# Optimization experiments

Hardware: AMD Instinct MI355X
Metric: run time of the kernel (lower is better)

Reference implementation:

```python
import jax, jax.numpy as jnp
import numpy as np

B, H, W, C, HEADS = 8, 64, 64, 128, 4
H_SP, W_SP = 64, 8            # idx=0: H_sp = H, W_sp = split_size
HD = C // HEADS               # 32
N = H_SP * W_SP               # 512 tokens per window
SCALE = HD ** -0.5


def setup_inputs() -> dict:
    key = jax.random.key(0)
    k1, k2, k3 = jax.random.split(key, 3)
    return {
        "qkv": jax.random.normal(k1, (3, B, H * W, C), dtype=jnp.float32),
        "conv_w": jax.random.normal(k2, (C, 1, 3, 3), dtype=jnp.float32) * 0.1,
        "conv_b": jax.random.normal(k3, (C,), dtype=jnp.float32) * 0.1,
    }


def _to_windows(x):
    # x: [B, L, C] -> window tokens [Bw, N, C] with Bw = B * (H//H_SP) * (W//W_SP)
    x = x.reshape(B, H // H_SP, H_SP, W // W_SP, W_SP, C)
    x = x.transpose(0, 1, 3, 2, 4, 5).reshape(-1, N, C)
    return x


def _heads(x):
    # [Bw, N, C] -> [Bw, heads, N, hd]
    return x.reshape(-1, N, HEADS, HD).transpose(0, 2, 1, 3)


def reference(qkv, conv_w, conv_b):
    q, k, v = qkv[0], qkv[1], qkv[2]

    qw = _heads(_to_windows(q)) * SCALE   # [Bw, h, N, hd]
    kw = _heads(_to_windows(k))

    vwin = _to_windows(v)                 # [Bw, N, C]
    # LePE: depthwise 3x3 conv on each window (NHWC, feature_group_count=C)
    vimg = vwin.reshape(-1, H_SP, W_SP, C)
    w_hwio = conv_w.transpose(2, 3, 1, 0)  # [3,3,1,C]
    lepe = jax.lax.conv_general_dilated(
        vimg, w_hwio, window_strides=(1, 1), padding='SAME',
        dimension_numbers=('NHWC', 'HWIO', 'NHWC'), feature_group_count=C,
    ) + conv_b
    lepe = _heads(lepe.reshape(-1, N, C))  # [Bw, h, N, hd]
    vw = _heads(vwin)

    attn = jax.nn.softmax(jnp.einsum('whqd,whkd->whqk', qw, kw), axis=-1)
    out = jnp.einsum('whqk,whkd->whqd', attn, vw) + lepe  # [Bw, h, N, hd]

    # merge heads and windows back to [B, L, C]
    out = out.transpose(0, 2, 1, 3).reshape(-1, N, C)
    out = out.reshape(B, H // H_SP, W // W_SP, H_SP, W_SP, C)
    out = out.transpose(0, 1, 3, 2, 4, 5).reshape(B, H * W, C)
    return out
```

## Files before the change

kernel.cpp:

```cpp
#include <hip/hip_runtime.h>


namespace {
constexpr int Bn   = 8;
constexpr int Ww   = 64;
constexpr int Cc   = 128;
constexpr int HD   = 32;
constexpr int WSP  = 8;
constexpr int NTOK = 512;
constexpr int LL   = 64 * 64;
constexpr float SCALE_L2E = 0.17677669529663687f * 1.4426950408889634f;
constexpr int KPAD = 40;
constexpr int VPAD = 536;
}

typedef __bf16 bf16x8 __attribute__((ext_vector_type(8)));
typedef float  f32x16 __attribute__((ext_vector_type(16)));
typedef unsigned int uint32x4 __attribute__((ext_vector_type(4)));

__device__ inline unsigned cvtpk(float x, float y) {
    unsigned r;
    asm("v_cvt_pk_bf16_f32 %0, %1, %2" : "=v"(r) : "v"(x), "v"(y));
    return r;
}

__global__ __launch_bounds__(1024, 4) void attn_kernel(const float* __restrict__ qkv,
                                                       const float* __restrict__ cw,
                                                       const float* __restrict__ cb,
                                                       float* __restrict__ out) {
    const int blk = blockIdx.x;
    const int w   = blk >> 2;
    const int h   = blk & 3;
    const int b   = w >> 3;
    const int wb  = w & 7;
    const int tid = threadIdx.x;
    const int wv  = tid >> 6;
    const int lane = tid & 63;
    const int l31 = lane & 31;
    const int h5  = lane >> 5;

    const float* qp = qkv;
    const float* kp = qkv + (size_t)Bn * LL * Cc;
    const float* vp = qkv + (size_t)2 * Bn * LL * Cc;

    __shared__ short K_lds[NTOK][KPAD];
    __shared__ short VT_lds[HD][VPAD];

    const int qtok = wv * 32 + l31;
    const int qlqi = (qtok >> 3) * Ww + wb * WSP + (qtok & 7);
    bf16x8 qf[2];
    {
        const float* p = qp + ((size_t)b * LL + qlqi) * Cc + h * HD + h5 * 8;
#pragma unroll
        for (int dc = 0; dc < 2; ++dc) {
            float4 a = *reinterpret_cast<const float4*>(p + dc * 16);
            float4 c = *reinterpret_cast<const float4*>(p + dc * 16 + 4);
            uint32x4 u;
            u.x = cvtpk(a.x * SCALE_L2E, a.y * SCALE_L2E);
            u.y = cvtpk(a.z * SCALE_L2E, a.w * SCALE_L2E);
            u.z = cvtpk(c.x * SCALE_L2E, c.y * SCALE_L2E);
            u.w = cvtpk(c.z * SCALE_L2E, c.w * SCALE_L2E);
            qf[dc] = __builtin_bit_cast(bf16x8, u);
        }
    }

    for (int i = tid; i < (NTOK / 2) * 8; i += 1024) {
        const int tp = i >> 3, j = i & 7;
        const int t0 = tp * 2, t1 = t0 + 1;
        const int lqi0 = (t0 >> 3) * Ww + wb * WSP + (t0 & 7);
        const size_t b0 = ((size_t)b * LL + lqi0) * Cc + h * HD + j * 4;
        const float4 k0 = *reinterpret_cast<const float4*>(kp + b0);
        const float4 k1 = *reinterpret_cast<const float4*>(kp + b0 + Cc);
        uint2 pk0, pk1;
        pk0.x = cvtpk(k0.x, k0.y);  pk0.y = cvtpk(k0.z, k0.w);
        pk1.x = cvtpk(k1.x, k1.y);  pk1.y = cvtpk(k1.z, k1.w);
        *reinterpret_cast<uint2*>(&K_lds[t0][j * 4]) = pk0;
        *reinterpret_cast<uint2*>(&K_lds[t1][j * 4]) = pk1;
        const float4 v0 = *reinterpret_cast<const float4*>(vp + b0);
        const float4 v1 = *reinterpret_cast<const float4*>(vp + b0 + Cc);
        *reinterpret_cast<unsigned*>(&VT_lds[j * 4 + 0][t0]) = cvtpk(v0.x, v1.x);
        *reinterpret_cast<unsigned*>(&VT_lds[j * 4 + 1][t0]) = cvtpk(v0.y, v1.y);
        *reinterpret_cast<unsigned*>(&VT_lds[j * 4 + 2][t0]) = cvtpk(v0.z, v1.z);
        *reinterpret_cast<unsigned*>(&VT_lds[j * 4 + 3][t0]) = cvtpk(v0.w, v1.w);
    }
    __syncthreads();

    f32x16 acc = (f32x16)(0.f);
    float lsum = 0.f;
    const f32x16 z16 = (f32x16)(0.f);

    auto load_kf = [&](int kt, bf16x8* kf) {
        const int krow = kt * 32 + l31;
#pragma unroll
        for (int dc = 0; dc < 2; ++dc)
            kf[dc] = __builtin_bit_cast(bf16x8,
                *reinterpret_cast<const uint32x4*>(&K_lds[krow][dc * 16 + h5 * 8]));
    };

    bf16x8 kf[2];
    load_kf(0, kf);

    for (int kt = 0; kt < 16; ++kt) {
        __builtin_amdgcn_s_setprio(1);
        f32x16 s = z16;
        s = __builtin_amdgcn_mfma_f32_32x32x16_bf16(kf[0], qf[0], s, 0, 0, 0);
        s = __builtin_amdgcn_mfma_f32_32x32x16_bf16(kf[1], qf[1], s, 0, 0, 0);
        __builtin_amdgcn_s_setprio(0);

        bf16x8 kfn[2];
        load_kf((kt + 1) & 15, kfn);
        uint32x4 vu[2];
#pragma unroll
        for (int kw = 0; kw < 2; ++kw) {
            const int kcol = kt * 32 + kw * 16 + h5 * 8;
            vu[kw] = *reinterpret_cast<const uint32x4*>(&VT_lds[l31][kcol]);
        }

        float pe[16];
#pragma unroll
        for (int i = 0; i < 16; ++i) pe[i] = __builtin_amdgcn_exp2f(s[i]);
        {
            float t0 = 0.f, t1 = 0.f;
#pragma unroll
            for (int i = 0; i < 8; ++i) { t0 += pe[2 * i]; t1 += pe[2 * i + 1]; }
            lsum += t0 + t1;
        }
        unsigned dw[8];
#pragma unroll
        for (int i = 0; i < 8; ++i) dw[i] = cvtpk(pe[2 * i], pe[2 * i + 1]);

#pragma unroll
        for (int kw = 0; kw < 2; ++kw) {
            unsigned a0 = dw[4 * kw + 0], b0 = dw[4 * kw + 2];
            unsigned a1 = dw[4 * kw + 1], b1 = dw[4 * kw + 3];
            asm("v_permlane32_swap_b32 %0, %1" : "+v"(a0), "+v"(b0));
            asm("v_permlane32_swap_b32 %0, %1" : "+v"(a1), "+v"(b1));
            uint32x4 pu; pu.x = a0; pu.y = a1; pu.z = b0; pu.w = b1;
            __builtin_amdgcn_s_setprio(1);
            acc = __builtin_amdgcn_mfma_f32_32x32x16_bf16(
                __builtin_bit_cast(bf16x8, pu), __builtin_bit_cast(bf16x8, vu[kw]),
                acc, 0, 0, 0);
            __builtin_amdgcn_s_setprio(0);
        }
        kf[0] = kfn[0];
        kf[1] = kfn[1];
    }

    lsum += __shfl_xor(lsum, 32);
    const float inv = 1.f / lsum;

    const int ch = h * HD + l31;
    float wreg[9];
#pragma unroll
    for (int wi = 0; wi < 9; ++wi) wreg[wi] = cw[ch * 9 + wi];
    const float bias = cb[ch];

    const int tok0 = wv * 32;
    unsigned hw[26];
    {
        const int segbase = tok0 + 4 * h5 - 12;
#pragma unroll
        for (int c2 = 0; c2 < 13; ++c2) {
            int t = segbase + 4 * c2;
            t = t < 0 ? 0 : (t > NTOK - 4 ? NTOK - 4 : t);
            const uint2 u = *reinterpret_cast<const uint2*>(&VT_lds[l31][t]);
            hw[c2 * 2 + 0] = u.x;
            hw[c2 * 2 + 1] = u.y;
        }
    }

#pragma unroll
    for (int r = 0; r < 16; ++r) {
        const int c_r = (r & 3) + 8 * (r >> 2);
        const float iv = __shfl(inv, c_r + 4 * h5);
        const int tok = tok0 + c_r + 4 * h5;
        float cv = bias;
#pragma unroll
        for (int dy = -1; dy <= 1; ++dy) {
            const bool rowok = (unsigned)(tok + dy * 8) < (unsigned)NTOK;
#pragma unroll
            for (int dx = -1; dx <= 1; ++dx) {
                const int idx = c_r + 12 + dy * 8 + dx;
                const unsigned word = hw[idx >> 1];
                const float tap = __builtin_bit_cast(float,
                    (idx & 1) ? (word & 0xFFFF0000u) : (word << 16));
                bool ok = rowok;
                if (dx == -1) ok = ok && (((r & 3) != 0) || (h5 != 0));
                if (dx == +1) ok = ok && (((r & 3) != 3) || (h5 == 0));
                cv += ok ? wreg[(dy + 1) * 3 + (dx + 1)] * tap : 0.f;
            }
        }
        const int lqi = (tok >> 3) * Ww + wb * WSP + (tok & 7);
        out[((size_t)b * LL + lqi) * Cc + ch] = acc[r] * iv + cv;
    }
}

extern "C" void kernel_launch(void* const* d_in, const int* in_sizes, int n_in,
                              void* d_out, int out_size, void* d_ws, size_t ws_size,
                              hipStream_t stream) {
    const float* qkv = (const float*)d_in[0];
    const float* cw  = (const float*)d_in[1];
    const float* cb  = (const float*)d_in[2];
    float* out = (float*)d_out;

    attn_kernel<<<256, 1024, 0, stream>>>(qkv, cw, cb, out);
}
```

Baseline: 29.19 us.

## Software-pipeline QK^T MFMA one tile ahead of softmax and PV

Restructures the key loop so the QK^T MFMAs for tile kt+1 are issued before the exp2/convert/PV work for tile kt, with K fragments loaded two tiles ahead. A sched_barrier pins the ordering, and the priority toggles around the PV MFMAs are dropped. The aim is to let the matrix unit overlap with the VALU exp work within each wave. The cost is extra live registers for the second score accumulator, which may hurt occupancy at 1024 threads per block. The last iterations compute wrapped-around scores that are never used.

```diff
diff --git a/kernel.cpp b/kernel.cpp
--- a/kernel.cpp
+++ b/kernel.cpp
@@ -97,28 +97,31 @@
                 *reinterpret_cast<const uint32x4*>(&K_lds[krow][dc * 16 + h5 * 8]));
     };
 
-    bf16x8 kf[2];
-    load_kf(0, kf);
+    bf16x8 kfA[2], kfB[2];
+    load_kf(0, kfA);
+    f32x16 s_cur = z16;
+    s_cur = __builtin_amdgcn_mfma_f32_32x32x16_bf16(kfA[0], qf[0], s_cur, 0, 0, 0);
+    s_cur = __builtin_amdgcn_mfma_f32_32x32x16_bf16(kfA[1], qf[1], s_cur, 0, 0, 0);
+    load_kf(1, kfB);
 
     for (int kt = 0; kt < 16; ++kt) {
         __builtin_amdgcn_s_setprio(1);
-        f32x16 s = z16;
-        s = __builtin_amdgcn_mfma_f32_32x32x16_bf16(kf[0], qf[0], s, 0, 0, 0);
-        s = __builtin_amdgcn_mfma_f32_32x32x16_bf16(kf[1], qf[1], s, 0, 0, 0);
+        f32x16 s_next = z16;
+        s_next = __builtin_amdgcn_mfma_f32_32x32x16_bf16(kfB[0], qf[0], s_next, 0, 0, 0);
+        s_next = __builtin_amdgcn_mfma_f32_32x32x16_bf16(kfB[1], qf[1], s_next, 0, 0, 0);
         __builtin_amdgcn_s_setprio(0);
-
-        bf16x8 kfn[2];
-        load_kf((kt + 1) & 15, kfn);
-        uint32x4 vu[2];
-#pragma unroll
-        for (int kw = 0; kw < 2; ++kw) {
-            const int kcol = kt * 32 + kw * 16 + h5 * 8;
-            vu[kw] = *reinterpret_cast<const uint32x4*>(&VT_lds[l31][kcol]);
-        }
+        load_kf((kt + 2) & 15, kfB);
+        uint32x4 vu0, vu1;
+        {
+            const int kcol = kt * 32 + h5 * 8;
+            vu0 = *reinterpret_cast<const uint32x4*>(&VT_lds[l31][kcol]);
+            vu1 = *reinterpret_cast<const uint32x4*>(&VT_lds[l31][kcol + 16]);
+        }
+        __builtin_amdgcn_sched_barrier(0);
 
         float pe[16];
 #pragma unroll
-        for (int i = 0; i < 16; ++i) pe[i] = __builtin_amdgcn_exp2f(s[i]);
+        for (int i = 0; i < 16; ++i) pe[i] = __builtin_amdgcn_exp2f(s_cur[i]);
         {
             float t0 = 0.f, t1 = 0.f;
 #pragma unroll
@@ -129,21 +132,25 @@
 #pragma unroll
         for (int i = 0; i < 8; ++i) dw[i] = cvtpk(pe[2 * i], pe[2 * i + 1]);
 
-#pragma unroll
-        for (int kw = 0; kw < 2; ++kw) {
-            unsigned a0 = dw[4 * kw + 0], b0 = dw[4 * kw + 2];
-            unsigned a1 = dw[4 * kw + 1], b1 = dw[4 * kw + 3];
+        {
+            unsigned a0 = dw[0], b0 = dw[2], a1 = dw[1], b1 = dw[3];
             asm("v_permlane32_swap_b32 %0, %1" : "+v"(a0), "+v"(b0));
             asm("v_permlane32_swap_b32 %0, %1" : "+v"(a1), "+v"(b1));
             uint32x4 pu; pu.x = a0; pu.y = a1; pu.z = b0; pu.w = b1;
-            __builtin_amdgcn_s_setprio(1);
             acc = __builtin_amdgcn_mfma_f32_32x32x16_bf16(
-                __builtin_bit_cast(bf16x8, pu), __builtin_bit_cast(bf16x8, vu[kw]),
+                __builtin_bit_cast(bf16x8, pu), __builtin_bit_cast(bf16x8, vu0),
                 acc, 0, 0, 0);
-            __builtin_amdgcn_s_setprio(0);
-        }
-        kf[0] = kfn[0];
-        kf[1] = kfn[1];
+        }
+        {
+            unsigned a0 = dw[4], b0 = dw[6], a1 = dw[5], b1 = dw[7];
+            asm("v_permlane32_swap_b32 %0, %1" : "+v"(a0), "+v"(b0));
+            asm("v_permlane32_swap_b32 %0, %1" : "+v"(a1), "+v"(b1));
+            uint32x4 pu; pu.x = a0; pu.y = a1; pu.z = b0; pu.w = b1;
+            acc = __builtin_amdgcn_mfma_f32_32x32x16_bf16(
+                __builtin_bit_cast(bf16x8, pu), __builtin_bit_cast(bf16x8, vu1),
+                acc, 0, 0, 0);
+        }
+        s_cur = s_next;
     }
 
     lsum += __shfl_xor(lsum, 32);
```

After: 30.89 us. 5.9% more time.

## Split keys across wave pairs and queries across two blocks per head

Applied to the files above, without the earlier changes.

Doubles the grid so each block handles half the query tokens of a window-head, and splits the key loop between two waves per query tile. Partial PV accumulators and row sums from the second wave are reduced through LDS (reusing the K buffer) before the LePE epilogue. This aims to raise parallelism and occupancy on the GPU, at the cost of duplicating the K/V staging per block and adding barriers plus an LDS reduction.

```diff
diff --git a/kernel.cpp b/kernel.cpp
--- a/kernel.cpp
+++ b/kernel.cpp
@@ -24,17 +24,20 @@
     return r;
 }
 
-__global__ __launch_bounds__(1024, 4) void attn_kernel(const float* __restrict__ qkv,
+__global__ __launch_bounds__(1024, 8) void attn_kernel(const float* __restrict__ qkv,
                                                        const float* __restrict__ cw,
                                                        const float* __restrict__ cb,
                                                        float* __restrict__ out) {
     const int blk = blockIdx.x;
-    const int w   = blk >> 2;
-    const int h   = blk & 3;
+    const int w   = blk >> 3;
+    const int h   = (blk >> 1) & 3;
+    const int qh  = blk & 1;
     const int b   = w >> 3;
     const int wb  = w & 7;
     const int tid = threadIdx.x;
-    const int wv  = tid >> 6;
+    const int wv   = tid >> 6;
+    const int pair = wv >> 1;
+    const int half = wv & 1;
     const int lane = tid & 63;
     const int l31 = lane & 31;
     const int h5  = lane >> 5;
@@ -46,7 +49,7 @@
     __shared__ short K_lds[NTOK][KPAD];
     __shared__ short VT_lds[HD][VPAD];
 
-    const int qtok = wv * 32 + l31;
+    const int qtok = qh * 256 + pair * 32 + l31;
     const int qlqi = (qtok >> 3) * Ww + wb * WSP + (qtok & 7);
     bf16x8 qf[2];
     {
@@ -97,10 +100,11 @@
                 *reinterpret_cast<const uint32x4*>(&K_lds[krow][dc * 16 + h5 * 8]));
     };
 
+    const int kt0 = half * 8;
     bf16x8 kf[2];
-    load_kf(0, kf);
-
-    for (int kt = 0; kt < 16; ++kt) {
+    load_kf(kt0, kf);
+
+    for (int kt = kt0; kt < kt0 + 8; ++kt) {
         __builtin_amdgcn_s_setprio(1);
         f32x16 s = z16;
         s = __builtin_amdgcn_mfma_f32_32x32x16_bf16(kf[0], qf[0], s, 0, 0, 0);
@@ -147,7 +151,28 @@
     }
 
     lsum += __shfl_xor(lsum, 32);
+
+    float* accbuf = reinterpret_cast<float*>(&K_lds[0][0]);
+    float* lsbuf  = accbuf + 8 * 32 * 32;
+    __syncthreads();
+    if (half == 1) {
+#pragma unroll
+        for (int r = 0; r < 16; ++r) {
+            const int c_r = (r & 3) + 8 * (r >> 2);
+            accbuf[(pair * 32 + c_r + 4 * h5) * 32 + l31] = acc[r];
+        }
+        if (lane < 32) lsbuf[pair * 32 + l31] = lsum;
+    }
+    __syncthreads();
+    if (half == 1) return;
+
+    lsum += lsbuf[pair * 32 + l31];
     const float inv = 1.f / lsum;
+#pragma unroll
+    for (int r = 0; r < 16; ++r) {
+        const int c_r = (r & 3) + 8 * (r >> 2);
+        acc[r] += accbuf[(pair * 32 + c_r + 4 * h5) * 32 + l31];
+    }
 
     const int ch = h * HD + l31;
     float wreg[9];
@@ -155,7 +180,7 @@
     for (int wi = 0; wi < 9; ++wi) wreg[wi] = cw[ch * 9 + wi];
     const float bias = cb[ch];
 
-    const int tok0 = wv * 32;
+    const int tok0 = qh * 256 + pair * 32;
     unsigned hw[26];
     {
         const int segbase = tok0 + 4 * h5 - 12;
@@ -203,5 +228,5 @@
     const float* cb  = (const float*)d_in[2];
     float* out = (float*)d_out;
 
-    attn_kernel<<<256, 1024, 0, stream>>>(qkv, cw, cb, out);
-}
+    attn_kernel<<<512, 1024, 0, stream>>>(qkv, cw, cb, out);
+}
```

Result: slower. 37.50 us (+28.5%).

## Split query tokens across two blocks and compute softmax row sums via MFMA

Applied to the files above, without the earlier changes.

The launch goes from 256 blocks of 1024 threads to 512 blocks of 512 threads, each handling half the query tokens of a (window, head) pair. The aim is more blocks across the CUs and a shorter per-block critical path. As a cost, each block now redundantly stages the full K and V tiles into LDS, doubling global reads of K/V. Softmax denominators are now produced by an extra MFMA against a vector of ones, which replaces the scalar add reduction and the cross-lane shuffle. The change also prefetches V fragments one iteration ahead and removes the setprio hints.

```diff
diff --git a/kernel.cpp b/kernel.cpp
--- a/kernel.cpp
+++ b/kernel.cpp
@@ -24,13 +24,14 @@
     return r;
 }
 
-__global__ __launch_bounds__(1024, 4) void attn_kernel(const float* __restrict__ qkv,
-                                                       const float* __restrict__ cw,
-                                                       const float* __restrict__ cb,
-                                                       float* __restrict__ out) {
+__global__ __launch_bounds__(512, 4) void attn_kernel(const float* __restrict__ qkv,
+                                                      const float* __restrict__ cw,
+                                                      const float* __restrict__ cb,
+                                                      float* __restrict__ out) {
     const int blk = blockIdx.x;
-    const int w   = blk >> 2;
-    const int h   = blk & 3;
+    const int w   = blk >> 3;
+    const int h   = (blk >> 1) & 3;
+    const int qh  = blk & 1;
     const int b   = w >> 3;
     const int wb  = w & 7;
     const int tid = threadIdx.x;
@@ -46,7 +47,7 @@
     __shared__ short K_lds[NTOK][KPAD];
     __shared__ short VT_lds[HD][VPAD];
 
-    const int qtok = wv * 32 + l31;
+    const int qtok = qh * 256 + wv * 32 + l31;
     const int qlqi = (qtok >> 3) * Ww + wb * WSP + (qtok & 7);
     bf16x8 qf[2];
     {
@@ -64,7 +65,7 @@
         }
     }
 
-    for (int i = tid; i < (NTOK / 2) * 8; i += 1024) {
+    for (int i = tid; i < (NTOK / 2) * 8; i += 512) {
         const int tp = i >> 3, j = i & 7;
         const int t0 = tp * 2, t1 = t0 + 1;
         const int lqi0 = (t0 >> 3) * Ww + wb * WSP + (t0 & 7);
@@ -85,9 +86,14 @@
     }
     __syncthreads();
 
-    f32x16 acc = (f32x16)(0.f);
-    float lsum = 0.f;
+    f32x16 acc  = (f32x16)(0.f);
+    f32x16 lacc = (f32x16)(0.f);
     const f32x16 z16 = (f32x16)(0.f);
+
+    uint32x4 onesu;
+    onesu.x = 0x3F803F80u; onesu.y = 0x3F803F80u;
+    onesu.z = 0x3F803F80u; onesu.w = 0x3F803F80u;
+    const bf16x8 onesf = __builtin_bit_cast(bf16x8, onesu);
 
     auto load_kf = [&](int kt, bf16x8* kf) {
         const int krow = kt * 32 + l31;
@@ -96,35 +102,32 @@
             kf[dc] = __builtin_bit_cast(bf16x8,
                 *reinterpret_cast<const uint32x4*>(&K_lds[krow][dc * 16 + h5 * 8]));
     };
+    auto load_vu = [&](int kt, uint32x4* vu) {
+#pragma unroll
+        for (int kw = 0; kw < 2; ++kw) {
+            const int kcol = kt * 32 + kw * 16 + h5 * 8;
+            vu[kw] = *reinterpret_cast<const uint32x4*>(&VT_lds[l31][kcol]);
+        }
+    };
 
     bf16x8 kf[2];
+    uint32x4 vu[2];
     load_kf(0, kf);
+    load_vu(0, vu);
 
     for (int kt = 0; kt < 16; ++kt) {
-        __builtin_amdgcn_s_setprio(1);
         f32x16 s = z16;
         s = __builtin_amdgcn_mfma_f32_32x32x16_bf16(kf[0], qf[0], s, 0, 0, 0);
         s = __builtin_amdgcn_mfma_f32_32x32x16_bf16(kf[1], qf[1], s, 0, 0, 0);
-        __builtin_amdgcn_s_setprio(0);
 
         bf16x8 kfn[2];
+        uint32x4 vun[2];
         load_kf((kt + 1) & 15, kfn);
-        uint32x4 vu[2];
-#pragma unroll
-        for (int kw = 0; kw < 2; ++kw) {
-            const int kcol = kt * 32 + kw * 16 + h5 * 8;
-            vu[kw] = *reinterpret_cast<const uint32x4*>(&VT_lds[l31][kcol]);
-        }
+        load_vu((kt + 1) & 15, vun);
 
         float pe[16];
 #pragma unroll
         for (int i = 0; i < 16; ++i) pe[i] = __builtin_amdgcn_exp2f(s[i]);
-        {
-            float t0 = 0.f, t1 = 0.f;
-#pragma unroll
-            for (int i = 0; i < 8; ++i) { t0 += pe[2 * i]; t1 += pe[2 * i + 1]; }
-            lsum += t0 + t1;
-        }
         unsigned dw[8];
 #pragma unroll
         for (int i = 0; i < 8; ++i) dw[i] = cvtpk(pe[2 * i], pe[2 * i + 1]);
@@ -136,18 +139,17 @@
             asm("v_permlane32_swap_b32 %0, %1" : "+v"(a0), "+v"(b0));
             asm("v_permlane32_swap_b32 %0, %1" : "+v"(a1), "+v"(b1));
             uint32x4 pu; pu.x = a0; pu.y = a1; pu.z = b0; pu.w = b1;
-            __builtin_amdgcn_s_setprio(1);
-            acc = __builtin_amdgcn_mfma_f32_32x32x16_bf16(
-                __builtin_bit_cast(bf16x8, pu), __builtin_bit_cast(bf16x8, vu[kw]),
-                acc, 0, 0, 0);
-            __builtin_amdgcn_s_setprio(0);
+            const bf16x8 pf = __builtin_bit_cast(bf16x8, pu);
+            acc  = __builtin_amdgcn_mfma_f32_32x32x16_bf16(
+                pf, __builtin_bit_cast(bf16x8, vu[kw]), acc, 0, 0, 0);
+            lacc = __builtin_amdgcn_mfma_f32_32x32x16_bf16(
+                pf, onesf, lacc, 0, 0, 0);
         }
         kf[0] = kfn[0];
         kf[1] = kfn[1];
-    }
-
-    lsum += __shfl_xor(lsum, 32);
-    const float inv = 1.f / lsum;
+        vu[0] = vun[0];
+        vu[1] = vun[1];
+    }
 
     const int ch = h * HD + l31;
     float wreg[9];
@@ -155,7 +157,7 @@
     for (int wi = 0; wi < 9; ++wi) wreg[wi] = cw[ch * 9 + wi];
     const float bias = cb[ch];
 
-    const int tok0 = wv * 32;
+    const int tok0 = qh * 256 + wv * 32;
     unsigned hw[26];
     {
         const int segbase = tok0 + 4 * h5 - 12;
@@ -172,7 +174,7 @@
 #pragma unroll
     for (int r = 0; r < 16; ++r) {
         const int c_r = (r & 3) + 8 * (r >> 2);
-        const float iv = __shfl(inv, c_r + 4 * h5);
+        const float iv = __builtin_amdgcn_rcpf(lacc[r]);
         const int tok = tok0 + c_r + 4 * h5;
         float cv = bias;
 #pragma unroll
@@ -203,5 +205,5 @@
     const float* cb  = (const float*)d_in[2];
     float* out = (float*)d_out;
 
-    attn_kernel<<<256, 1024, 0, stream>>>(qkv, cw, cb, out);
-}
+    attn_kernel<<<512, 512, 0, stream>>>(qkv, cw, cb, out);
+}
```

Measured after the change: 32.08 us. 9.9% more time.
